# Optimization experiments

Measured on AMD Instinct MI355X. Metric: run time of the kernel, lower is better.

The kernel has to match this reference:

```python
import jax, jax.numpy as jnp
import numpy as np


def _forward(x, conv_w, conv_b, lin_w, lin_b, W_in, conv1d_w, conv1d_b, W_x, W_dt, b_dt, A_log, Dp, W_out, We, be, Wa, ba, Wq, bq):
    B, _, H, Wd = x.shape
    E = conv_w.shape[0]
    # conv stem: Conv2d(k=3, pad=1) -> flatten(2) -> Linear(H*W -> img_size)
    z = jax.lax.conv_general_dilated(x, conv_w, (1, 1), [(1, 1), (1, 1)],
                                     dimension_numbers=('NCHW', 'OIHW', 'NCHW'))
    z = z + conv_b[None, :, None, None]
    z = z.reshape(B, E, H * Wd)                              # [B,E,HW]
    z = jnp.einsum('ben,mn->bem', z, lin_w) + lin_b          # [B,E,L]
    u = z.transpose(2, 0, 1)                                 # [L,B,E]: Mamba sees batch=L, seq=B
    # ---- Mamba block (mamba_ssm reference math) ----
    di = W_in.shape[0] // 2
    xz = u @ W_in.T                                          # [L,seq,2*di]
    xm, zg = xz[..., :di], xz[..., di:]
    K = conv1d_w.shape[-1]
    xc = jax.lax.conv_general_dilated(xm.transpose(0, 2, 1), conv1d_w, (1,), [(K - 1, 0)],
                                      dimension_numbers=('NCH', 'OIH', 'NCH'),
                                      feature_group_count=di)  # causal depthwise conv
    xs = jax.nn.silu((xc + conv1d_b[None, :, None]).transpose(0, 2, 1))  # [L,seq,di]
    dbl = xs @ W_x.T                                         # [L,seq,dt_rank+2S]
    dt_rank = W_dt.shape[1]
    S = A_log.shape[1]
    delta = jax.nn.softplus(dbl[..., :dt_rank] @ W_dt.T + b_dt)          # [L,seq,di]
    Bm = dbl[..., dt_rank:dt_rank + S]                       # [L,seq,S]
    Cm = dbl[..., dt_rank + S:]                              # [L,seq,S]
    A = -jnp.exp(A_log)                                      # [di,S]

    def step(h, t):
        d_t, b_t, c_t, x_t = t                               # [L,di],[L,S],[L,S],[L,di]
        h = jnp.exp(d_t[:, :, None] * A) * h + (d_t * x_t)[:, :, None] * b_t[:, None, :]
        return h, jnp.einsum('lds,ls->ld', h, c_t)

    h0 = jnp.zeros((u.shape[0], di, S), xs.dtype)
    _, ys = jax.lax.scan(step, h0, (delta.transpose(1, 0, 2), Bm.transpose(1, 0, 2),
                                    Cm.transpose(1, 0, 2), xs.transpose(1, 0, 2)))
    y = (ys.transpose(1, 0, 2) + xs * Dp) * jax.nn.silu(zg)  # [L,seq,di]
    out = y @ W_out.T                                        # [L,seq,E]
    feat = out[-1]                                           # [B,E] (last 'mamba batch' row)
    return feat @ We.T + be, feat @ Wa.T + ba, feat @ Wq.T + bq


def setup_inputs() -> dict:
    key = jax.random.key(0)
    ks = jax.random.split(key, 16)
    B, C, IMG, E, S, K = 512, 1, 32, 128, 256, 4
    di, dt_rank = 2 * E, 8
    sc = 0.02
    return {
        'x': jax.random.normal(ks[0], (B, C, IMG, IMG), jnp.float32),
        'conv_w': sc * jax.random.normal(ks[1], (E, C, 3, 3), jnp.float32),
        'conv_b': jnp.zeros((E,), jnp.float32),
        'lin_w': sc * jax.random.normal(ks[2], (IMG, IMG * IMG), jnp.float32),
        'lin_b': jnp.zeros((IMG,), jnp.float32),
        'W_in': sc * jax.random.normal(ks[3], (2 * di, E), jnp.float32),
        'conv1d_w': sc * jax.random.normal(ks[4], (di, 1, K), jnp.float32),
        'conv1d_b': jnp.zeros((di,), jnp.float32),
        'W_x': sc * jax.random.normal(ks[5], (dt_rank + 2 * S, di), jnp.float32),
        'W_dt': sc * jax.random.normal(ks[6], (di, dt_rank), jnp.float32),
        'b_dt': 0.1 * jax.random.normal(ks[7], (di,), jnp.float32),
        'A_log': jnp.log(jnp.broadcast_to(jnp.arange(1, S + 1, dtype=jnp.float32), (di, S))),
        'Dp': jnp.ones((di,), jnp.float32),
        'W_out': sc * jax.random.normal(ks[8], (E, di), jnp.float32),
        'We': sc * jax.random.normal(ks[9], (1, E), jnp.float32),
        'be': jnp.zeros((1,), jnp.float32),
        'Wa': sc * jax.random.normal(ks[10], (3, E), jnp.float32),
        'ba': jnp.zeros((3,), jnp.float32),
        'Wq': sc * jax.random.normal(ks[11], (4, E), jnp.float32),
        'bq': jnp.zeros((4,), jnp.float32),
    }


def reference(x, conv_w, conv_b, lin_w, lin_b, W_in, conv1d_w, conv1d_b, W_x, W_dt, b_dt, A_log, Dp, W_out, We, be, Wa, ba, Wq, bq):
    return _forward(x, conv_w, conv_b, lin_w, lin_b, W_in, conv1d_w, conv1d_b, W_x,
                    W_dt, b_dt, A_log, Dp, W_out, We, be, Wa, ba, Wq, bq)
```

## Files before the change

### kernel.cpp

```cpp
#include <hip/hip_runtime.h>
#include <math.h>

#define BATCH 512
#define E     128
#define DI    256
#define S     256
#define DTR   8
#define KCONV 4
#define JWX   520
#define NC    32
#define TCV   (BATCH / NC)

__device__ __forceinline__ float silu_f(float v) {
    return v / (1.0f + __expf(-v));
}

__global__ __launch_bounds__(256) void kA_pre(
    const float* __restrict__ x, const float* __restrict__ conv_w,
    const float* __restrict__ conv_b, const float* __restrict__ lin_w,
    const float* __restrict__ lin_b, const float* __restrict__ W_in,
    const float* __restrict__ W_x, const float* __restrict__ W_out,
    float* __restrict__ xm, float* __restrict__ zg,
    float* __restrict__ W_xT, float* __restrict__ W_outT)
{
    const int tid = threadIdx.x;
    if (blockIdx.x >= 512) {
        const int bid = blockIdx.x - 512;
        const float* src; float* dst; int J, K, j0;
        if (bid < 9) { src = W_x;   dst = W_xT;   J = JWX; K = DI; j0 = bid * 64; }
        else         { src = W_out; dst = W_outT; J = E;   K = DI; j0 = (bid - 9) * 64; }
        const int j = j0 + (tid & 63);
        if (j >= J) return;
        for (int c = tid >> 6; c < K; c += 4)
            dst[c * J + j] = src[j * K + c];
        return;
    }

    const int b = blockIdx.x;
    __shared__ float lw[1024];
    __shared__ float red[10][4];
    __shared__ float Tsh[10];
    __shared__ float u[E];

    const float4 lv = ((const float4*)(lin_w + 31 * 1024))[tid];
    ((float4*)lw)[tid] = lv;
    __syncthreads();

    float acc[10];
#pragma unroll
    for (int k = 0; k < 10; k++) acc[k] = 0.0f;

    const float4 xv = ((const float4*)(x + (size_t)b * 1024))[tid];
    const int p0 = tid * 4;
    const int h = p0 >> 5, w0 = p0 & 31;
    const float xa[4] = {xv.x, xv.y, xv.z, xv.w};
#pragma unroll
    for (int k = 0; k < 4; k++) {
        const float xval = xa[k];
        const int w = w0 + k;
#pragma unroll
        for (int i = 0; i < 3; i++) {
            const int hh = h - (i - 1);
            if (hh < 0 || hh > 31) continue;
#pragma unroll
            for (int j = 0; j < 3; j++) {
                const int ww = w - (j - 1);
                if (ww < 0 || ww > 31) continue;
                acc[i * 3 + j] += xval * lw[hh * 32 + ww];
            }
        }
    }
    acc[9] = lv.x + lv.y + lv.z + lv.w;

    const int wv = tid >> 6, ln = tid & 63;
#pragma unroll
    for (int k = 0; k < 10; k++) {
#pragma unroll
        for (int m = 1; m < 64; m <<= 1) acc[k] += __shfl_xor(acc[k], m, 64);
    }
    if (ln == 0) {
#pragma unroll
        for (int k = 0; k < 10; k++) red[k][wv] = acc[k];
    }
    __syncthreads();
    if (tid < 10) Tsh[tid] = red[tid][0] + red[tid][1] + red[tid][2] + red[tid][3];
    __syncthreads();

    if (tid < E) {
        const int e = tid;
        float v = lin_b[31] + conv_b[e] * Tsh[9];
#pragma unroll
        for (int k = 0; k < 9; k++) v += conv_w[e * 9 + k] * Tsh[k];
        u[e] = v;
    }
    __syncthreads();

    {
        const float4* w0p = (const float4*)(W_in + (size_t)tid * E);
        const float4* w1p = (const float4*)(W_in + (size_t)(tid + 256) * E);
        float a0 = 0.0f;
#pragma unroll 8
        for (int e4 = 0; e4 < E / 4; e4++) {
            const float4 w = w0p[e4];
            a0 += u[4*e4]*w.x + u[4*e4+1]*w.y + u[4*e4+2]*w.z + u[4*e4+3]*w.w;
        }
        float a1 = 0.0f;
#pragma unroll 8
        for (int e4 = 0; e4 < E / 4; e4++) {
            const float4 w = w1p[e4];
            a1 += u[4*e4]*w.x + u[4*e4+1]*w.y + u[4*e4+2]*w.z + u[4*e4+3]*w.w;
        }
        xm[b * DI + tid] = a0;
        zg[b * DI + tid] = a1;
    }
}

__global__ __launch_bounds__(256) void k2b_conv_wx(
    const float* __restrict__ xm, const float* __restrict__ c1w,
    const float* __restrict__ conv1d_b, const float* __restrict__ W_xT,
    const float* __restrict__ W_dt, const float* __restrict__ b_dt,
    float* __restrict__ xs_g, float* __restrict__ delta_g,
    float* __restrict__ Bm, float* __restrict__ Cm)
{
    const int bb = blockIdx.x * 4;
    const int g = blockIdx.y;
    const int tid = threadIdx.x;
    __shared__ float xs[4][DI];
    __shared__ float dtin[4][8];

    for (int idx = tid; idx < 4 * DI; idx += 256) {
        const int r = idx >> 8, c = idx & 255;
        const int b = bb + r;
        const float4 wc = ((const float4*)c1w)[c];
        float a = conv1d_b[c];
        if (b >= 3) a += xm[(b - 3) * DI + c] * wc.x;
        if (b >= 2) a += xm[(b - 2) * DI + c] * wc.y;
        if (b >= 1) a += xm[(b - 1) * DI + c] * wc.z;
        a += xm[b * DI + c] * wc.w;
        const float s = silu_f(a);
        xs[r][c] = s;
        if (g == 0) xs_g[b * DI + c] = s;
    }
    __syncthreads();

    const int r = tid >> 6;
    const int j = g * 64 + (tid & 63);
    if (j < JWX) {
        float a = 0.0f;
#pragma unroll 8
        for (int c = 0; c < DI; c++) a += xs[r][c] * W_xT[c * JWX + j];
        const int b = bb + r;
        if (j < DTR)          dtin[r][j] = a;
        else if (j < DTR + S) Bm[b * S + (j - DTR)] = a;
        else                  Cm[b * S + (j - DTR - S)] = a;
    }
    __syncthreads();

    if (g == 0) {
        const int d = tid;
        const float bd = b_dt[d];
        const float4 wd0 = ((const float4*)(W_dt + d * DTR))[0];
        const float4 wd1 = ((const float4*)(W_dt + d * DTR))[1];
#pragma unroll
        for (int r2 = 0; r2 < 4; r2++) {
            float a = bd
                + dtin[r2][0]*wd0.x + dtin[r2][1]*wd0.y + dtin[r2][2]*wd0.z + dtin[r2][3]*wd0.w
                + dtin[r2][4]*wd1.x + dtin[r2][5]*wd1.y + dtin[r2][6]*wd1.z + dtin[r2][7]*wd1.w;
            const float sp = (a > 20.0f) ? a : log1pf(__expf(a));
            delta_g[(bb + r2) * DI + d] = sp;
        }
    }
}

__global__ __launch_bounds__(256) void k3u_up(
    const float* __restrict__ A_log, const float* __restrict__ delta,
    const float* __restrict__ xs, const float* __restrict__ Bm,
    float* __restrict__ hloc, float* __restrict__ Dchunk)
{
    const int tid = threadIdx.x;
    const int wv = tid >> 6, ln = tid & 63;
    const int d = blockIdx.x * 4 + wv;
    const int c = blockIdx.y;
    const int s0 = ln * 4;
    const int t0 = c * TCV;

    const float4 al = *(const float4*)(A_log + d * S + s0);
    float4 A;
    A.x = -__expf(al.x); A.y = -__expf(al.y);
    A.z = -__expf(al.z); A.w = -__expf(al.w);

    float4 h = make_float4(0.f, 0.f, 0.f, 0.f);
    float cd = 0.0f;
    for (int tb = 0; tb < TCV; tb += 8) {
#pragma unroll
        for (int i = 0; i < 8; i++) {
            const int tt = t0 + tb + i;
            const float dd = delta[tt * DI + d];
            cd += dd;
            const float u = dd * xs[tt * DI + d];
            const float4 B = *(const float4*)(Bm + tt * S + s0);
            h.x = __expf(dd * A.x) * h.x + u * B.x;
            h.y = __expf(dd * A.y) * h.y + u * B.y;
            h.z = __expf(dd * A.z) * h.z + u * B.z;
            h.w = __expf(dd * A.w) * h.w + u * B.w;
        }
    }
    *(float4*)(hloc + ((size_t)(c * DI + d)) * S + s0) = h;
    if (ln == 0) Dchunk[c * DI + d] = cd;
}

__global__ __launch_bounds__(256) void k3d_down(
    const float* __restrict__ A_log, const float* __restrict__ delta,
    const float* __restrict__ xs, const float* __restrict__ Bm,
    const float* __restrict__ Cm, const float* __restrict__ hloc,
    const float* __restrict__ Dchunk, float* __restrict__ y)
{
    const int tid = threadIdx.x;
    const int wv = tid >> 6, ln = tid & 63;
    const int d = blockIdx.x * 4 + wv;
    const int c = (NC - 1) - blockIdx.y;
    const int s0 = ln * 4;
    const int t0 = c * TCV;

    const float4 al = *(const float4*)(A_log + d * S + s0);
    float4 A;
    A.x = -__expf(al.x); A.y = -__expf(al.y);
    A.z = -__expf(al.z); A.w = -__expf(al.w);

    float4 h = make_float4(0.f, 0.f, 0.f, 0.f);
    for (int cp = 1; cp <= c; cp++) {
        const float4 hl = *(const float4*)(hloc + ((size_t)((cp - 1) * DI + d)) * S + s0);
        const float Dc = Dchunk[(cp - 1) * DI + d];
        h.x = hl.x + __expf(A.x * Dc) * h.x;
        h.y = hl.y + __expf(A.y * Dc) * h.y;
        h.z = hl.z + __expf(A.z * Dc) * h.z;
        h.w = hl.w + __expf(A.w * Dc) * h.w;
    }

    float pr[8];
    for (int tb = 0; tb < TCV; tb += 8) {
#pragma unroll
        for (int i = 0; i < 8; i++) {
            const int tt = t0 + tb + i;
            const float dd = delta[tt * DI + d];
            const float u = dd * xs[tt * DI + d];
            const float4 B = *(const float4*)(Bm + tt * S + s0);
            const float4 C = *(const float4*)(Cm + tt * S + s0);
            h.x = __expf(dd * A.x) * h.x + u * B.x;
            h.y = __expf(dd * A.y) * h.y + u * B.y;
            h.z = __expf(dd * A.z) * h.z + u * B.z;
            h.w = __expf(dd * A.w) * h.w + u * B.w;
            pr[i] = h.x * C.x + h.y * C.y + h.z * C.z + h.w * C.w;
        }

        float q0, q1, q2, q3;
        {
            const bool b0 = (ln & 1);
            float s_, r_;
            s_ = b0 ? pr[0] : pr[1]; r_ = __shfl_xor(s_, 1, 64);
            q0 = (b0 ? pr[1] : pr[0]) + r_;
            s_ = b0 ? pr[2] : pr[3]; r_ = __shfl_xor(s_, 1, 64);
            q1 = (b0 ? pr[3] : pr[2]) + r_;
            s_ = b0 ? pr[4] : pr[5]; r_ = __shfl_xor(s_, 1, 64);
            q2 = (b0 ? pr[5] : pr[4]) + r_;
            s_ = b0 ? pr[6] : pr[7]; r_ = __shfl_xor(s_, 1, 64);
            q3 = (b0 ? pr[7] : pr[6]) + r_;
        }
        {
            const bool b1 = (ln & 2);
            float s_, r_;
            s_ = b1 ? q0 : q1; r_ = __shfl_xor(s_, 2, 64);
            q0 = (b1 ? q1 : q0) + r_;
            s_ = b1 ? q2 : q3; r_ = __shfl_xor(s_, 2, 64);
            q1 = (b1 ? q3 : q2) + r_;
        }
        {
            const bool b2 = (ln & 4);
            const float s_ = b2 ? q0 : q1;
            const float r_ = __shfl_xor(s_, 4, 64);
            q0 = (b2 ? q1 : q0) + r_;
        }
        q0 += __shfl_xor(q0, 8, 64);
        q0 += __shfl_xor(q0, 16, 64);
        q0 += __shfl_xor(q0, 32, 64);
        if (ln < 8) y[(t0 + tb + ln) * DI + d] = q0;
    }
}

__global__ __launch_bounds__(256) void k4_heads(
    const float* __restrict__ y, const float* __restrict__ xs,
    const float* __restrict__ Dp, const float* __restrict__ zg,
    const float* __restrict__ W_outT,
    const float* __restrict__ We, const float* __restrict__ be,
    const float* __restrict__ Wa, const float* __restrict__ ba,
    const float* __restrict__ Wq, const float* __restrict__ bq,
    float* __restrict__ out)
{
    const int bb = blockIdx.x * 2;
    const int tid = threadIdx.x;
    __shared__ float yf[2][DI];
    __shared__ float feat[2][E];

    for (int idx = tid; idx < 2 * DI; idx += 256) {
        const int r = idx >> 8, c = idx & 255;
        const int b = bb + r;
        const float z = zg[b * DI + c];
        yf[r][c] = (y[b * DI + c] + xs[b * DI + c] * Dp[c]) * silu_f(z);
    }
    __syncthreads();

    {
        const int r = tid >> 7, e = tid & 127;
        float a = 0.0f;
#pragma unroll 8
        for (int dd = 0; dd < DI; dd++) a += yf[r][dd] * W_outT[dd * E + e];
        feat[r][e] = a;
    }
    __syncthreads();

    if (tid < 16) {
        const int r = tid >> 3, hd = tid & 7;
        const int b = bb + r;
        const float* wrow;
        float bias;
        int dst;
        if (hd == 0)      { wrow = We;                 bias = be[0];      dst = b; }
        else if (hd < 4)  { wrow = Wa + (hd - 1) * E;  bias = ba[hd - 1]; dst = 512 + b * 3 + (hd - 1); }
        else              { wrow = Wq + (hd - 4) * E;  bias = bq[hd - 4]; dst = 2048 + b * 4 + (hd - 4); }
        float a = bias;
#pragma unroll 4
        for (int e = 0; e < E; e++) a += feat[r][e] * wrow[e];
        out[dst] = a;
    }
}

extern "C" void kernel_launch(void* const* d_in, const int* in_sizes, int n_in,
                              void* d_out, int out_size, void* d_ws, size_t ws_size,
                              hipStream_t stream)
{
    const float* x        = (const float*)d_in[0];
    const float* conv_w   = (const float*)d_in[1];
    const float* conv_b   = (const float*)d_in[2];
    const float* lin_w    = (const float*)d_in[3];
    const float* lin_b    = (const float*)d_in[4];
    const float* W_in     = (const float*)d_in[5];
    const float* conv1d_w = (const float*)d_in[6];
    const float* conv1d_b = (const float*)d_in[7];
    const float* W_x      = (const float*)d_in[8];
    const float* W_dt     = (const float*)d_in[9];
    const float* b_dt     = (const float*)d_in[10];
    const float* A_log    = (const float*)d_in[11];
    const float* Dp       = (const float*)d_in[12];
    const float* W_out    = (const float*)d_in[13];
    const float* We       = (const float*)d_in[14];
    const float* be       = (const float*)d_in[15];
    const float* Wa       = (const float*)d_in[16];
    const float* ba       = (const float*)d_in[17];
    const float* Wq       = (const float*)d_in[18];
    const float* bq       = (const float*)d_in[19];
    float* out = (float*)d_out;

    float* ws = (float*)d_ws;
    float* xm     = ws;
    float* zg     = xm     + 512 * 256;
    float* xs     = zg     + 512 * 256;
    float* delta  = xs     + 512 * 256;
    float* Bm     = delta  + 512 * 256;
    float* Cm     = Bm     + 512 * 256;
    float* y      = Cm     + 512 * 256;
    float* W_xT   = y      + 512 * 256;
    float* W_outT = W_xT   + 256 * JWX;
    float* hloc   = W_outT + 256 * 128;
    float* Dchunk = hloc   + (size_t)NC * DI * S;

    kA_pre<<<523, 256, 0, stream>>>(x, conv_w, conv_b, lin_w, lin_b,
                                    W_in, W_x, W_out, xm, zg, W_xT, W_outT);
    k2b_conv_wx<<<dim3(128, 9), 256, 0, stream>>>(xm, conv1d_w, conv1d_b, W_xT,
                                                  W_dt, b_dt, xs, delta, Bm, Cm);
    k3u_up<<<dim3(64, NC), 256, 0, stream>>>(A_log, delta, xs, Bm, hloc, Dchunk);
    k3d_down<<<dim3(64, NC), 256, 0, stream>>>(A_log, delta, xs, Bm, Cm,
                                               hloc, Dchunk, y);
    k4_heads<<<256, 256, 0, stream>>>(y, xs, Dp, zg, W_outT, We, be, Wa, ba, Wq, bq, out);
}
```

Measured before the change: 182.8 us.

## Drop weight transposes; read W_x and W_out rows directly with float4 dot products

Removes the in-kernel transposition of W_x and W_out into workspace. k2b and k4 now compute each output as a row dot product over the original row-major weights, using float4 loads against shared activations. k2b is regridded so each thread handles two batch rows across half of the 520 outputs, which cuts the grid from 9 to 4 y-blocks. The stem's 10 separate wave reductions are replaced by a butterfly transpose-reduce that needs fewer shuffles. In exchange, per-thread row reads are strided across lanes (uncoalesced) and rely on cache.

```diff
diff --git a/kernel.cpp b/kernel.cpp
--- a/kernel.cpp
+++ b/kernel.cpp
@@ -19,23 +19,9 @@
     const float* __restrict__ x, const float* __restrict__ conv_w,
     const float* __restrict__ conv_b, const float* __restrict__ lin_w,
     const float* __restrict__ lin_b, const float* __restrict__ W_in,
-    const float* __restrict__ W_x, const float* __restrict__ W_out,
-    float* __restrict__ xm, float* __restrict__ zg,
-    float* __restrict__ W_xT, float* __restrict__ W_outT)
+    float* __restrict__ xm, float* __restrict__ zg)
 {
     const int tid = threadIdx.x;
-    if (blockIdx.x >= 512) {
-        const int bid = blockIdx.x - 512;
-        const float* src; float* dst; int J, K, j0;
-        if (bid < 9) { src = W_x;   dst = W_xT;   J = JWX; K = DI; j0 = bid * 64; }
-        else         { src = W_out; dst = W_outT; J = E;   K = DI; j0 = (bid - 9) * 64; }
-        const int j = j0 + (tid & 63);
-        if (j >= J) return;
-        for (int c = tid >> 6; c < K; c += 4)
-            dst[c * J + j] = src[j * K + c];
-        return;
-    }
-
     const int b = blockIdx.x;
     __shared__ float lw[1024];
     __shared__ float red[10][4];
@@ -73,15 +59,49 @@
     acc[9] = lv.x + lv.y + lv.z + lv.w;
 
     const int wv = tid >> 6, ln = tid & 63;
-#pragma unroll
-    for (int k = 0; k < 10; k++) {
-#pragma unroll
-        for (int m = 1; m < 64; m <<= 1) acc[k] += __shfl_xor(acc[k], m, 64);
-    }
-    if (ln == 0) {
-#pragma unroll
-        for (int k = 0; k < 10; k++) red[k][wv] = acc[k];
-    }
+
+    float R0, q4;
+    {
+        float q0, q1, q2, q3;
+        {
+            const bool b0 = (ln & 1);
+            float s_, r_;
+            s_ = b0 ? acc[0] : acc[1]; r_ = __shfl_xor(s_, 1, 64);
+            q0 = (b0 ? acc[1] : acc[0]) + r_;
+            s_ = b0 ? acc[2] : acc[3]; r_ = __shfl_xor(s_, 1, 64);
+            q1 = (b0 ? acc[3] : acc[2]) + r_;
+            s_ = b0 ? acc[4] : acc[5]; r_ = __shfl_xor(s_, 1, 64);
+            q2 = (b0 ? acc[5] : acc[4]) + r_;
+            s_ = b0 ? acc[6] : acc[7]; r_ = __shfl_xor(s_, 1, 64);
+            q3 = (b0 ? acc[7] : acc[6]) + r_;
+            s_ = b0 ? acc[8] : acc[9]; r_ = __shfl_xor(s_, 1, 64);
+            q4 = (b0 ? acc[9] : acc[8]) + r_;
+        }
+        {
+            const bool b1 = (ln & 2);
+            float s_, r_;
+            s_ = b1 ? q0 : q1; r_ = __shfl_xor(s_, 2, 64);
+            q0 = (b1 ? q1 : q0) + r_;
+            s_ = b1 ? q2 : q3; r_ = __shfl_xor(s_, 2, 64);
+            q1 = (b1 ? q3 : q2) + r_;
+            q4 += __shfl_xor(q4, 2, 64);
+        }
+        {
+            const bool b2 = (ln & 4);
+            const float s_ = b2 ? q0 : q1;
+            const float r_ = __shfl_xor(s_, 4, 64);
+            R0 = (b2 ? q1 : q0) + r_;
+            q4 += __shfl_xor(q4, 4, 64);
+        }
+        R0 += __shfl_xor(R0, 8, 64);
+        R0 += __shfl_xor(R0, 16, 64);
+        R0 += __shfl_xor(R0, 32, 64);
+        q4 += __shfl_xor(q4, 8, 64);
+        q4 += __shfl_xor(q4, 16, 64);
+        q4 += __shfl_xor(q4, 32, 64);
+    }
+    if (ln < 8) red[ln][wv] = R0;
+    if (ln < 2) red[8 + ln][wv] = q4;
     __syncthreads();
     if (tid < 10) Tsh[tid] = red[tid][0] + red[tid][1] + red[tid][2] + red[tid][3];
     __syncthreads();
@@ -117,16 +137,18 @@
 
 __global__ __launch_bounds__(256) void k2b_conv_wx(
     const float* __restrict__ xm, const float* __restrict__ c1w,
-    const float* __restrict__ conv1d_b, const float* __restrict__ W_xT,
+    const float* __restrict__ conv1d_b, const float* __restrict__ W_x,
     const float* __restrict__ W_dt, const float* __restrict__ b_dt,
     float* __restrict__ xs_g, float* __restrict__ delta_g,
     float* __restrict__ Bm, float* __restrict__ Cm)
 {
     const int bb = blockIdx.x * 4;
-    const int g = blockIdx.y;
+    const int gy = blockIdx.y;
+    const int jhalf = gy >> 1;
+    const int rp = (gy & 1) * 2;
     const int tid = threadIdx.x;
-    __shared__ float xs[4][DI];
-    __shared__ float dtin[4][8];
+    __shared__ float xs_sh[4][DI];
+    __shared__ float dtin[2][8];
 
     for (int idx = tid; idx < 4 * DI; idx += 256) {
         const int r = idx >> 8, c = idx & 255;
@@ -138,36 +160,50 @@
         if (b >= 1) a += xm[(b - 1) * DI + c] * wc.z;
         a += xm[b * DI + c] * wc.w;
         const float s = silu_f(a);
-        xs[r][c] = s;
-        if (g == 0) xs_g[b * DI + c] = s;
-    }
-    __syncthreads();
-
-    const int r = tid >> 6;
-    const int j = g * 64 + (tid & 63);
-    if (j < JWX) {
-        float a = 0.0f;
+        xs_sh[r][c] = s;
+        if (gy == 0) xs_g[b * DI + c] = s;
+    }
+    __syncthreads();
+
+    for (int jl = tid; jl < 260; jl += 256) {
+        const int jj = jhalf * 260 + jl;
+        const float4* wr = (const float4*)(W_x + (size_t)jj * DI);
+        const float4* xA = (const float4*)xs_sh[rp];
+        const float4* xB = (const float4*)xs_sh[rp + 1];
+        float a0 = 0.0f, a1 = 0.0f;
 #pragma unroll 8
-        for (int c = 0; c < DI; c++) a += xs[r][c] * W_xT[c * JWX + j];
-        const int b = bb + r;
-        if (j < DTR)          dtin[r][j] = a;
-        else if (j < DTR + S) Bm[b * S + (j - DTR)] = a;
-        else                  Cm[b * S + (j - DTR - S)] = a;
-    }
-    __syncthreads();
-
-    if (g == 0) {
+        for (int c4 = 0; c4 < 64; c4++) {
+            const float4 w  = wr[c4];
+            const float4 vA = xA[c4];
+            const float4 vB = xB[c4];
+            a0 += vA.x * w.x; a0 += vA.y * w.y; a0 += vA.z * w.z; a0 += vA.w * w.w;
+            a1 += vB.x * w.x; a1 += vB.y * w.y; a1 += vB.z * w.z; a1 += vB.w * w.w;
+        }
+        const int b0 = bb + rp, b1 = bb + rp + 1;
+        if (jj < DTR) {
+            dtin[0][jj] = a0; dtin[1][jj] = a1;
+        } else if (jj < DTR + S) {
+            Bm[b0 * S + (jj - DTR)] = a0;
+            Bm[b1 * S + (jj - DTR)] = a1;
+        } else {
+            Cm[b0 * S + (jj - DTR - S)] = a0;
+            Cm[b1 * S + (jj - DTR - S)] = a1;
+        }
+    }
+    __syncthreads();
+
+    if (jhalf == 0) {
         const int d = tid;
         const float bd = b_dt[d];
         const float4 wd0 = ((const float4*)(W_dt + d * DTR))[0];
         const float4 wd1 = ((const float4*)(W_dt + d * DTR))[1];
 #pragma unroll
-        for (int r2 = 0; r2 < 4; r2++) {
+        for (int r2 = 0; r2 < 2; r2++) {
             float a = bd
                 + dtin[r2][0]*wd0.x + dtin[r2][1]*wd0.y + dtin[r2][2]*wd0.z + dtin[r2][3]*wd0.w
                 + dtin[r2][4]*wd1.x + dtin[r2][5]*wd1.y + dtin[r2][6]*wd1.z + dtin[r2][7]*wd1.w;
             const float sp = (a > 20.0f) ? a : log1pf(__expf(a));
-            delta_g[(bb + r2) * DI + d] = sp;
+            delta_g[(bb + rp + r2) * DI + d] = sp;
         }
     }
 }
@@ -290,7 +326,7 @@
 __global__ __launch_bounds__(256) void k4_heads(
     const float* __restrict__ y, const float* __restrict__ xs,
     const float* __restrict__ Dp, const float* __restrict__ zg,
-    const float* __restrict__ W_outT,
+    const float* __restrict__ W_out,
     const float* __restrict__ We, const float* __restrict__ be,
     const float* __restrict__ Wa, const float* __restrict__ ba,
     const float* __restrict__ Wq, const float* __restrict__ bq,
@@ -311,9 +347,15 @@
 
     {
         const int r = tid >> 7, e = tid & 127;
+        const float4* wr = (const float4*)(W_out + (size_t)e * DI);
+        const float4* yv = (const float4*)yf[r];
         float a = 0.0f;
 #pragma unroll 8
-        for (int dd = 0; dd < DI; dd++) a += yf[r][dd] * W_outT[dd * E + e];
+        for (int d4 = 0; d4 < 64; d4++) {
+            const float4 w = wr[d4];
+            const float4 v = yv[d4];
+            a += v.x * w.x; a += v.y * w.y; a += v.z * w.z; a += v.w * w.w;
+        }
         feat[r][e] = a;
     }
     __syncthreads();
@@ -368,17 +410,15 @@
     float* Bm     = delta  + 512 * 256;
     float* Cm     = Bm     + 512 * 256;
     float* y      = Cm     + 512 * 256;
-    float* W_xT   = y      + 512 * 256;
-    float* W_outT = W_xT   + 256 * JWX;
-    float* hloc   = W_outT + 256 * 128;
+    float* hloc   = y      + 512 * 256;
     float* Dchunk = hloc   + (size_t)NC * DI * S;
 
-    kA_pre<<<523, 256, 0, stream>>>(x, conv_w, conv_b, lin_w, lin_b,
-                                    W_in, W_x, W_out, xm, zg, W_xT, W_outT);
-    k2b_conv_wx<<<dim3(128, 9), 256, 0, stream>>>(xm, conv1d_w, conv1d_b, W_xT,
+    kA_pre<<<512, 256, 0, stream>>>(x, conv_w, conv_b, lin_w, lin_b, W_in,
+                                    xm, zg);
+    k2b_conv_wx<<<dim3(128, 4), 256, 0, stream>>>(xm, conv1d_w, conv1d_b, W_x,
                                                   W_dt, b_dt, xs, delta, Bm, Cm);
     k3u_up<<<dim3(64, NC), 256, 0, stream>>>(A_log, delta, xs, Bm, hloc, Dchunk);
     k3d_down<<<dim3(64, NC), 256, 0, stream>>>(A_log, delta, xs, Bm, Cm,
                                                hloc, Dchunk, y);
-    k4_heads<<<256, 256, 0, stream>>>(y, xs, Dp, zg, W_outT, We, be, Wa, ba, Wq, bq, out);
-}
+    k4_heads<<<256, 256, 0, stream>>>(y, xs, Dp, zg, W_out, We, be, Wa, ba, Wq, bq, out);
+}
```

New measurement: 177.6 us. -2.8%, faster.
